# Kernel tuning notes

Hardware: AMD Instinct MI355X
Metric: run time of the kernel (lower is better)

## Reference

```python
import jax, jax.numpy as jnp
import numpy as np

N_SRC = 12000
N_TAR = 12000


def _make_points(key, n):
    p3 = jax.random.normal(key, (n, 3), dtype=jnp.float32) * 2.0
    return jnp.concatenate([p3, jnp.ones((n, 1), dtype=jnp.float32)], axis=1)  # homogeneous


def _make_covs(key, n):
    # SPD 3x3 blocks embedded into 4x4 covariances (row/col 3 are zero, as GICP covs)
    A = jax.random.normal(key, (n, 3, 3), dtype=jnp.float32) * 0.1
    c3 = jnp.einsum('nij,nkj->nik', A, A) + 0.01 * jnp.eye(3, dtype=jnp.float32)
    return jnp.zeros((n, 4, 4), dtype=jnp.float32).at[:, :3, :3].set(c3)


def setup_inputs() -> dict:
    key = jax.random.key(0)
    k1, k2, k3, k4 = jax.random.split(key, 4)
    return {
        'transformation': jnp.eye(4, dtype=jnp.float32),
        'src_points': _make_points(k1, N_SRC),
        'tar_points': _make_points(k2, N_TAR),
        'covs_src': _make_covs(k3, N_SRC),
        'covs_tar': _make_covs(k4, N_TAR),
    }


def reference(transformation, src_points, tar_points, covs_src, covs_tar):
    T = transformation
    # NN search uses points @ T.T (as in forward())
    tsrc = src_points @ T.T  # [N,4]
    # squared euclidean distances (argmin equivalent to cdist argmin)
    d2 = (jnp.sum(tsrc * tsrc, axis=1, keepdims=True)
          + jnp.sum(tar_points * tar_points, axis=1)[None, :]
          - 2.0 * (tsrc @ tar_points.T))  # [N_src, N_tar]
    idx = jnp.argmin(d2, axis=1)  # [N_src]

    # transformed source covariances: T @ C @ T^T
    tcov = jnp.einsum('ij,njk,lk->nil', T, covs_src, T)  # [N,4,4]
    comb3 = (covs_tar[idx] + tcov)[:, :3, :3]  # [N,3,3]
    inv3 = jnp.linalg.inv(comb3)

    # loss branch uses points @ T (faithful to source code)
    pT = src_points @ T  # [N,4]
    r = tar_points[idx, :3] - pT[:, :3]  # [N,3]
    mah = jnp.einsum('ni,nij,nj->n', r, inv3, r)  # per-point Mahalanobis
    return jnp.mean(mah)
```

## Files before the change

kernel.cpp:

```cpp
#include <hip/hip_runtime.h>
#include <math.h>

#define N_PTS 12000
#define NT_CHUNKS 150
#define CHUNK 80
#define SRC_PER_BLOCK 2048
#define SRC_BLOCKS 6
#define MAH_BLOCKS 47

__global__ __launch_bounds__(256) void nn_partial_kernel(
    const float* __restrict__ T,
    const float* __restrict__ src,
    const float* __restrict__ tar,
    float* __restrict__ pval,
    unsigned int* __restrict__ counter)
{
    __shared__ float4 lds[CHUNK];
    const int tid   = threadIdx.x;
    const int sblk  = blockIdx.x;
    const int chunk = blockIdx.y;
    const int jbase = chunk * CHUNK;

    if (sblk == 0 && chunk == 0 && tid == 0) atomicExch(counter, 0u);

    const float T00=T[0],  T01=T[1],  T02=T[2],  T03=T[3];
    const float T10=T[4],  T11=T[5],  T12=T[6],  T13=T[7];
    const float T20=T[8],  T21=T[9],  T22=T[10], T23=T[11];

    if (tid < CHUNK) {
        float4 t = ((const float4*)tar)[jbase + tid];
        float n3 = fmaf(t.x, t.x, fmaf(t.y, t.y, t.z * t.z));
        lds[tid] = make_float4(t.x, t.y, t.z, n3);
    }
    __syncthreads();

    float sx[8], sy[8], sz[8], mval[8];
    const int base = sblk * SRC_PER_BLOCK + tid;
    #pragma unroll
    for (int k = 0; k < 8; ++k) {
        int i = base + k * 256;
        if (i >= N_PTS) i = N_PTS - 1;
        float4 p = ((const float4*)src)[i];
        float tx = fmaf(T00, p.x, fmaf(T01, p.y, fmaf(T02, p.z, T03 * p.w)));
        float ty = fmaf(T10, p.x, fmaf(T11, p.y, fmaf(T12, p.z, T13 * p.w)));
        float tz = fmaf(T20, p.x, fmaf(T21, p.y, fmaf(T22, p.z, T23 * p.w)));
        sx[k] = -2.0f * tx;
        sy[k] = -2.0f * ty;
        sz[k] = -2.0f * tz;
        mval[k] = INFINITY;
    }

    #pragma unroll 4
    for (int j = 0; j < CHUNK; ++j) {
        const float4 t = lds[j];
        #pragma unroll
        for (int k = 0; k < 8; ++k) {
            float s = fmaf(sx[k], t.x, fmaf(sy[k], t.y, fmaf(sz[k], t.z, t.w)));
            mval[k] = fminf(mval[k], s);
        }
    }

    #pragma unroll
    for (int k = 0; k < 8; ++k) {
        int i = base + k * 256;
        if (i < N_PTS) pval[chunk * N_PTS + i] = mval[k];
    }
}

__global__ __launch_bounds__(256) void mah_finalize_kernel(
    const float* __restrict__ T,
    const float* __restrict__ src,
    const float* __restrict__ tar,
    const float* __restrict__ cs,
    const float* __restrict__ ct,
    const float* __restrict__ pval,
    float* __restrict__ bsum,
    unsigned int* __restrict__ counter,
    float* __restrict__ out)
{
    const int i = blockIdx.x * 256 + threadIdx.x;
    float mah = 0.0f;

    if (i < N_PTS) {
        float Tm[4][4];
        #pragma unroll
        for (int a = 0; a < 16; ++a) ((float*)Tm)[a] = T[a];

        float best = INFINITY; int bc = 0;
        #pragma unroll 10
        for (int c = 0; c < NT_CHUNKS; ++c) {
            float v = pval[c * N_PTS + i];
            if (v < best) { best = v; bc = c; }
        }

        float4 p = ((const float4*)src)[i];
        float tx = fmaf(Tm[0][0], p.x, fmaf(Tm[0][1], p.y, fmaf(Tm[0][2], p.z, Tm[0][3] * p.w)));
        float ty = fmaf(Tm[1][0], p.x, fmaf(Tm[1][1], p.y, fmaf(Tm[1][2], p.z, Tm[1][3] * p.w)));
        float tz = fmaf(Tm[2][0], p.x, fmaf(Tm[2][1], p.y, fmaf(Tm[2][2], p.z, Tm[2][3] * p.w)));
        const float sx = -2.0f * tx, sy = -2.0f * ty, sz = -2.0f * tz;

        const int jbase = bc * CHUNK;
        float best2 = INFINITY; int bidx = 0;
        #pragma unroll 8
        for (int j = 0; j < CHUNK; ++j) {
            float4 t = ((const float4*)tar)[jbase + j];
            float n3 = fmaf(t.x, t.x, fmaf(t.y, t.y, t.z * t.z));
            float s = fmaf(sx, t.x, fmaf(sy, t.y, fmaf(sz, t.z, n3)));
            if (s < best2) { best2 = s; bidx = jbase + j; }
        }

        float C[4][4];
        #pragma unroll
        for (int a = 0; a < 16; ++a) ((float*)C)[a] = cs[i * 16 + a];

        float B[4][3];
        #pragma unroll
        for (int j = 0; j < 4; ++j)
            #pragma unroll
            for (int c = 0; c < 3; ++c)
                B[j][c] = C[j][0]*Tm[c][0] + C[j][1]*Tm[c][1]
                        + C[j][2]*Tm[c][2] + C[j][3]*Tm[c][3];

        const float* ctb = ct + (size_t)bidx * 16;
        float M[3][3];
        #pragma unroll
        for (int r = 0; r < 3; ++r)
            #pragma unroll
            for (int c = 0; c < 3; ++c)
                M[r][c] = Tm[r][0]*B[0][c] + Tm[r][1]*B[1][c]
                        + Tm[r][2]*B[2][c] + Tm[r][3]*B[3][c]
                        + ctb[r * 4 + c];

        const float a_ = M[0][0], b_ = M[0][1], c_ = M[0][2];
        const float d_ = M[1][0], e_ = M[1][1], f_ = M[1][2];
        const float g_ = M[2][0], h_ = M[2][1], i_ = M[2][2];

        const float A0 = e_*i_ - f_*h_;
        const float A1 = f_*g_ - d_*i_;
        const float A2 = d_*h_ - e_*g_;
        const float det = a_*A0 + b_*A1 + c_*A2;
        const float rdet = 1.0f / det;

        float inv[3][3];
        inv[0][0] = A0 * rdet;
        inv[0][1] = (c_*h_ - b_*i_) * rdet;
        inv[0][2] = (b_*f_ - c_*e_) * rdet;
        inv[1][0] = A1 * rdet;
        inv[1][1] = (a_*i_ - c_*g_) * rdet;
        inv[1][2] = (c_*d_ - a_*f_) * rdet;
        inv[2][0] = A2 * rdet;
        inv[2][1] = (b_*g_ - a_*h_) * rdet;
        inv[2][2] = (a_*e_ - b_*d_) * rdet;

        float p0 = p.x*Tm[0][0] + p.y*Tm[1][0] + p.z*Tm[2][0] + p.w*Tm[3][0];
        float p1 = p.x*Tm[0][1] + p.y*Tm[1][1] + p.z*Tm[2][1] + p.w*Tm[3][1];
        float p2 = p.x*Tm[0][2] + p.y*Tm[1][2] + p.z*Tm[2][2] + p.w*Tm[3][2];

        const float4 tp = ((const float4*)tar)[bidx];
        const float r0 = tp.x - p0;
        const float r1 = tp.y - p1;
        const float r2 = tp.z - p2;

        mah = r0*(inv[0][0]*r0 + inv[0][1]*r1 + inv[0][2]*r2)
            + r1*(inv[1][0]*r0 + inv[1][1]*r1 + inv[1][2]*r2)
            + r2*(inv[2][0]*r0 + inv[2][1]*r1 + inv[2][2]*r2);
    }

    float v = mah;
    #pragma unroll
    for (int off = 32; off > 0; off >>= 1)
        v += __shfl_down(v, off, 64);

    __shared__ float wsum[4];
    __shared__ int lastflag;
    if ((threadIdx.x & 63) == 0) wsum[threadIdx.x >> 6] = v;
    __syncthreads();
    if (threadIdx.x == 0) {
        float tot = wsum[0] + wsum[1] + wsum[2] + wsum[3];
        atomicExch(&bsum[blockIdx.x], tot);
        __threadfence();
        unsigned int old = atomicAdd(counter, 1u);
        lastflag = (old == MAH_BLOCKS - 1) ? 1 : 0;
    }
    __syncthreads();

    if (lastflag && threadIdx.x < 64) {
        __threadfence();
        double acc = 0.0;
        if (threadIdx.x < MAH_BLOCKS)
            acc = (double)atomicAdd(&bsum[threadIdx.x], 0.0f);
        #pragma unroll
        for (int off = 32; off > 0; off >>= 1)
            acc += __shfl_down(acc, off, 64);
        if (threadIdx.x == 0)
            out[0] = (float)(acc / (double)N_PTS);
    }
}

extern "C" void kernel_launch(void* const* d_in, const int* in_sizes, int n_in,
                              void* d_out, int out_size, void* d_ws, size_t ws_size,
                              hipStream_t stream) {
    const float* T   = (const float*)d_in[0];
    const float* src = (const float*)d_in[1];
    const float* tar = (const float*)d_in[2];
    const float* cs  = (const float*)d_in[3];
    const float* ct  = (const float*)d_in[4];
    float* out = (float*)d_out;

    char* ws = (char*)d_ws;
    unsigned int* counter = (unsigned int*)ws;
    float* bsum = (float*)(ws + 16);
    float* pval = (float*)(ws + 256);

    dim3 g1(SRC_BLOCKS, NT_CHUNKS);
    nn_partial_kernel<<<g1, 256, 0, stream>>>(T, src, tar, pval, counter);

    mah_finalize_kernel<<<MAH_BLOCKS, 256, 0, stream>>>(
        T, src, tar, cs, ct, pval, bsum, counter, out);
}
```

Baseline: 41.45 us.

## Split finalize per source point across four waves for chunk and rescan search

The finalize kernel now assigns 64 source points per block and spreads the 150-chunk minimum scan and the 80-candidate rescan across four waves. Partial results are merged through shared memory with lowest-index tie-breaking, and only wave 0 runs the covariance inversion and the reduction. This raises the block count from 47 to 188, so the serial per-thread latency chain in the finalize kernel is spread over more of the GPU. The cost is extra LDS traffic and block barriers, and the workspace offsets move to make room for the larger block-sum array.

```diff
diff --git a/kernel.cpp b/kernel.cpp
--- a/kernel.cpp
+++ b/kernel.cpp
@@ -6,7 +6,8 @@
 #define CHUNK 80
 #define SRC_PER_BLOCK 2048
 #define SRC_BLOCKS 6
-#define MAH_BLOCKS 47
+#define MAH_BLOCKS 188
+#define RES_PER_WAVE 20
 
 __global__ __launch_bounds__(256) void nn_partial_kernel(
     const float* __restrict__ T,
@@ -78,40 +79,67 @@
     unsigned int* __restrict__ counter,
     float* __restrict__ out)
 {
-    const int i = blockIdx.x * 256 + threadIdx.x;
-    float mah = 0.0f;
-
-    if (i < N_PTS) {
-        float Tm[4][4];
-        #pragma unroll
-        for (int a = 0; a < 16; ++a) ((float*)Tm)[a] = T[a];
-
-        float best = INFINITY; int bc = 0;
-        #pragma unroll 10
-        for (int c = 0; c < NT_CHUNKS; ++c) {
-            float v = pval[c * N_PTS + i];
-            if (v < best) { best = v; bc = c; }
-        }
-
-        float4 p = ((const float4*)src)[i];
-        float tx = fmaf(Tm[0][0], p.x, fmaf(Tm[0][1], p.y, fmaf(Tm[0][2], p.z, Tm[0][3] * p.w)));
-        float ty = fmaf(Tm[1][0], p.x, fmaf(Tm[1][1], p.y, fmaf(Tm[1][2], p.z, Tm[1][3] * p.w)));
-        float tz = fmaf(Tm[2][0], p.x, fmaf(Tm[2][1], p.y, fmaf(Tm[2][2], p.z, Tm[2][3] * p.w)));
-        const float sx = -2.0f * tx, sy = -2.0f * ty, sz = -2.0f * tz;
-
-        const int jbase = bc * CHUNK;
-        float best2 = INFINITY; int bidx = 0;
-        #pragma unroll 8
-        for (int j = 0; j < CHUNK; ++j) {
-            float4 t = ((const float4*)tar)[jbase + j];
-            float n3 = fmaf(t.x, t.x, fmaf(t.y, t.y, t.z * t.z));
-            float s = fmaf(sx, t.x, fmaf(sy, t.y, fmaf(sz, t.z, n3)));
-            if (s < best2) { best2 = s; bidx = jbase + j; }
+    __shared__ float lds_v[4][64];
+    __shared__ int   lds_i[4][64];
+
+    const int lane = threadIdx.x & 63;
+    const int wv   = threadIdx.x >> 6;
+    const int i    = blockIdx.x * 64 + lane;
+    const int ic   = (i < N_PTS) ? i : (N_PTS - 1);
+    const float4* tar4 = (const float4*)tar;
+
+    float bv = INFINITY; int bc = 0;
+    #pragma unroll 8
+    for (int c = wv; c < NT_CHUNKS; c += 4) {
+        float v = pval[c * N_PTS + ic];
+        if (v < bv) { bv = v; bc = c; }
+    }
+    lds_v[wv][lane] = bv;
+    lds_i[wv][lane] = bc;
+    __syncthreads();
+
+    float cv = lds_v[0][lane]; int cc = lds_i[0][lane];
+    #pragma unroll
+    for (int w = 1; w < 4; ++w) {
+        float v = lds_v[w][lane]; int c = lds_i[w][lane];
+        if (v < cv || (v == cv && c < cc)) { cv = v; cc = c; }
+    }
+    __syncthreads();
+
+    float Tm[4][4];
+    #pragma unroll
+    for (int a = 0; a < 16; ++a) ((float*)Tm)[a] = T[a];
+
+    const float4 p = ((const float4*)src)[ic];
+    const float tx = fmaf(Tm[0][0], p.x, fmaf(Tm[0][1], p.y, fmaf(Tm[0][2], p.z, Tm[0][3] * p.w)));
+    const float ty = fmaf(Tm[1][0], p.x, fmaf(Tm[1][1], p.y, fmaf(Tm[1][2], p.z, Tm[1][3] * p.w)));
+    const float tz = fmaf(Tm[2][0], p.x, fmaf(Tm[2][1], p.y, fmaf(Tm[2][2], p.z, Tm[2][3] * p.w)));
+    const float sx = -2.0f * tx, sy = -2.0f * ty, sz = -2.0f * tz;
+
+    const int jb = cc * CHUNK + wv * RES_PER_WAVE;
+    float rv = INFINITY; int rj = 0;
+    #pragma unroll 5
+    for (int jj = 0; jj < RES_PER_WAVE; ++jj) {
+        float4 t = tar4[jb + jj];
+        float n3 = fmaf(t.x, t.x, fmaf(t.y, t.y, t.z * t.z));
+        float s  = fmaf(sx, t.x, fmaf(sy, t.y, fmaf(sz, t.z, n3)));
+        if (s < rv) { rv = s; rj = jb + jj; }
+    }
+    lds_v[wv][lane] = rv;
+    lds_i[wv][lane] = rj;
+    __syncthreads();
+
+    if (wv == 0) {
+        float fv = lds_v[0][lane]; int bidx = lds_i[0][lane];
+        #pragma unroll
+        for (int w = 1; w < 4; ++w) {
+            float v = lds_v[w][lane]; int j = lds_i[w][lane];
+            if (v < fv || (v == fv && j < bidx)) { fv = v; bidx = j; }
         }
 
         float C[4][4];
         #pragma unroll
-        for (int a = 0; a < 16; ++a) ((float*)C)[a] = cs[i * 16 + a];
+        for (int a = 0; a < 16; ++a) ((float*)C)[a] = cs[ic * 16 + a];
 
         float B[4][3];
         #pragma unroll
@@ -152,48 +180,43 @@
         inv[2][1] = (b_*g_ - a_*h_) * rdet;
         inv[2][2] = (a_*e_ - b_*d_) * rdet;
 
-        float p0 = p.x*Tm[0][0] + p.y*Tm[1][0] + p.z*Tm[2][0] + p.w*Tm[3][0];
-        float p1 = p.x*Tm[0][1] + p.y*Tm[1][1] + p.z*Tm[2][1] + p.w*Tm[3][1];
-        float p2 = p.x*Tm[0][2] + p.y*Tm[1][2] + p.z*Tm[2][2] + p.w*Tm[3][2];
-
-        const float4 tp = ((const float4*)tar)[bidx];
+        const float p0 = p.x*Tm[0][0] + p.y*Tm[1][0] + p.z*Tm[2][0] + p.w*Tm[3][0];
+        const float p1 = p.x*Tm[0][1] + p.y*Tm[1][1] + p.z*Tm[2][1] + p.w*Tm[3][1];
+        const float p2 = p.x*Tm[0][2] + p.y*Tm[1][2] + p.z*Tm[2][2] + p.w*Tm[3][2];
+
+        const float4 tp = tar4[bidx];
         const float r0 = tp.x - p0;
         const float r1 = tp.y - p1;
         const float r2 = tp.z - p2;
 
-        mah = r0*(inv[0][0]*r0 + inv[0][1]*r1 + inv[0][2]*r2)
-            + r1*(inv[1][0]*r0 + inv[1][1]*r1 + inv[1][2]*r2)
-            + r2*(inv[2][0]*r0 + inv[2][1]*r1 + inv[2][2]*r2);
-    }
-
-    float v = mah;
-    #pragma unroll
-    for (int off = 32; off > 0; off >>= 1)
-        v += __shfl_down(v, off, 64);
-
-    __shared__ float wsum[4];
-    __shared__ int lastflag;
-    if ((threadIdx.x & 63) == 0) wsum[threadIdx.x >> 6] = v;
-    __syncthreads();
-    if (threadIdx.x == 0) {
-        float tot = wsum[0] + wsum[1] + wsum[2] + wsum[3];
-        atomicExch(&bsum[blockIdx.x], tot);
-        __threadfence();
-        unsigned int old = atomicAdd(counter, 1u);
-        lastflag = (old == MAH_BLOCKS - 1) ? 1 : 0;
-    }
-    __syncthreads();
-
-    if (lastflag && threadIdx.x < 64) {
-        __threadfence();
-        double acc = 0.0;
-        if (threadIdx.x < MAH_BLOCKS)
-            acc = (double)atomicAdd(&bsum[threadIdx.x], 0.0f);
+        float mah = r0*(inv[0][0]*r0 + inv[0][1]*r1 + inv[0][2]*r2)
+                  + r1*(inv[1][0]*r0 + inv[1][1]*r1 + inv[1][2]*r2)
+                  + r2*(inv[2][0]*r0 + inv[2][1]*r1 + inv[2][2]*r2);
+        if (i >= N_PTS) mah = 0.0f;
+
         #pragma unroll
         for (int off = 32; off > 0; off >>= 1)
-            acc += __shfl_down(acc, off, 64);
-        if (threadIdx.x == 0)
-            out[0] = (float)(acc / (double)N_PTS);
+            mah += __shfl_down(mah, off, 64);
+
+        unsigned int old = 0u;
+        if (lane == 0) {
+            bsum[blockIdx.x] = mah;
+            __threadfence();
+            old = atomicAdd(counter, 1u);
+        }
+        old = __shfl(old, 0, 64);
+
+        if (old == MAH_BLOCKS - 1) {
+            __threadfence();
+            double acc = 0.0;
+            for (int s = lane; s < MAH_BLOCKS; s += 64)
+                acc += (double)atomicAdd(&bsum[s], 0.0f);
+            #pragma unroll
+            for (int off = 32; off > 0; off >>= 1)
+                acc += __shfl_down(acc, off, 64);
+            if (lane == 0)
+                out[0] = (float)(acc / (double)N_PTS);
+        }
     }
 }
 
@@ -209,8 +232,8 @@
 
     char* ws = (char*)d_ws;
     unsigned int* counter = (unsigned int*)ws;
-    float* bsum = (float*)(ws + 16);
-    float* pval = (float*)(ws + 256);
+    float* bsum = (float*)(ws + 256);
+    float* pval = (float*)(ws + 4096);
 
     dim3 g1(SRC_BLOCKS, NT_CHUNKS);
     nn_partial_kernel<<<g1, 256, 0, stream>>>(T, src, tar, pval, counter);
```

Result: faster. 35.26 us (-14.9%).
